# Performance work log

Hardware: AMD Instinct MI355X
Metric: run time of the kernel (lower is better)

## Reference

```python
import jax, jax.numpy as jnp
import numpy as np

N_NODES = 50000
N_EDGES = 1600000
F_IN = 256
OUT = 64
HEADS = 8


def setup_inputs() -> dict:
    key = jax.random.key(0)
    ks = jax.random.split(key, 6)
    x = jax.random.normal(ks[0], (N_NODES, F_IN), dtype=jnp.float32)
    edge_row = jax.random.randint(ks[1], (N_EDGES,), 0, N_NODES, dtype=jnp.int32)
    edge_col = jax.random.randint(ks[2], (N_EDGES,), 0, N_NODES, dtype=jnp.int32)
    Ws = jax.random.normal(ks[3], (HEADS, OUT, F_IN), dtype=jnp.float32) * (1.0 / np.sqrt(F_IN))
    Ws_bias = jnp.zeros((HEADS, OUT), dtype=jnp.float32)
    As = jax.random.normal(ks[4], (HEADS, 2 * OUT, 1), dtype=jnp.float32) * (1.0 / np.sqrt(OUT))
    As_bias = jnp.zeros((HEADS, 2), dtype=jnp.float32)
    return {"x": x, "edge_row": edge_row, "edge_col": edge_col,
            "Ws": Ws, "Ws_bias": Ws_bias, "As": As, "As_bias": As_bias}


def reference(x, edge_row, edge_col, Ws, Ws_bias, As, As_bias):
    # GAT forward, inference mode (training=False -> dropout rates 0).
    # Graph is a binary symmetric adjacency given as an edge list; the original's
    # sparse add of row_partial + transpose(col_partial) reduces to per-edge
    # score(i,j) = Al[i] + b0 + Ar[j] + b1 for every edge (i,j).
    # NOTE: the original computes leaky_relu(E) but then softmaxes E (lrelu is
    # discarded); we faithfully reproduce that: softmax over raw scores.
    H, O, F = Ws.shape
    N = x.shape[0]
    t = jnp.einsum('nf,hof->hno', x, Ws)                      # [H,N,O] transformed nodes
    Al = jnp.einsum('hno,ho->hn', t, As[:, :O, 0]) + As_bias[:, 0:1]  # [H,N]
    Ar = jnp.einsum('hno,ho->hn', t, As[:, O:, 0]) + As_bias[:, 1:2]  # [H,N]
    scores = Al[:, edge_row] + Ar[:, edge_col]                 # [H,E]
    seg_max = jax.vmap(lambda s: jax.ops.segment_max(s, edge_row, num_segments=N))(scores)
    seg_max = jnp.where(jnp.isfinite(seg_max), seg_max, jnp.float32(0.0))
    ex = jnp.exp(scores - seg_max[:, edge_row])                # [H,E]
    denom = jax.vmap(lambda e: jax.ops.segment_sum(e, edge_row, num_segments=N))(ex)
    alpha = ex / denom[:, edge_row]                            # row-wise sparse softmax
    # per-head aggregation (loop over small fixed head count bounds memory)
    h = jnp.stack([
        jax.ops.segment_sum(alpha[k][:, None] * t[k, edge_col, :], edge_row, num_segments=N)
        for k in range(H)
    ])                                                         # [H,N,O]
    h = h + Ws_bias[:, None, :]
    out = jnp.transpose(h, (1, 0, 2)).reshape(N, H * O)        # concat heads (reduction=False)
    return jax.nn.elu(out)
```

## Files before the change

### kernel.cpp

```cpp
#include <hip/hip_runtime.h>
#include <hip/hip_fp16.h>

#define HEADS 8
#define F_IN 256
#define OUT 64
#define NOUT 512
#define CAP 1024
#define CAPP (CAP + 16)

#define RPB 128
#define MAXB 512
#define CHA 8192

typedef __attribute__((ext_vector_type(8))) _Float16 f16x8;
typedef __attribute__((ext_vector_type(2))) _Float16 f16x2;
typedef __attribute__((ext_vector_type(4))) float f32x4;

__device__ __forceinline__ short f2h(float f) {
  _Float16 h = (_Float16)f;
  return *(short*)&h;
}
__device__ __forceinline__ f16x2 u2h2(unsigned u) {
  union { unsigned u; f16x2 h; } x; x.u = u; return x.h;
}
__device__ __forceinline__ float h2f(unsigned short b) {
  _Float16 h = *(_Float16*)&b; return (float)h;
}

__global__ __launch_bounds__(256) void conv_kernel(
    const float* __restrict__ src, short* __restrict__ dst, int n8)
{
  int i = blockIdx.x * 256 + threadIdx.x;
  if (i >= n8) return;
  const float4 a = *(const float4*)(src + (size_t)i * 8);
  const float4 b = *(const float4*)(src + (size_t)i * 8 + 4);
  short r[8] = { f2h(a.x), f2h(a.y), f2h(a.z), f2h(a.w),
                 f2h(b.x), f2h(b.y), f2h(b.z), f2h(b.w) };
  *(uint4*)(dst + (size_t)i * 8) = *(uint4*)r;
}

__global__ __launch_bounds__(256) void va_kernel(
    const short* __restrict__ W2, const float* __restrict__ As,
    unsigned short* __restrict__ va16)
{
  const int h = blockIdx.x, k = threadIdx.x;
  const unsigned short* W = (const unsigned short*)W2;
  float s = 0.f;
  #pragma unroll 8
  for (int o = 0; o < OUT; ++o)
    s += h2f(W[(size_t)(h * OUT + o) * F_IN + k]) * As[h * 2 * OUT + OUT + o];
  va16[h * F_IN + k] = (unsigned short)f2h(s);
}

__global__ __launch_bounds__(256) void argemv_kernel(
    const short* __restrict__ xh, const unsigned short* __restrict__ va16,
    const float* __restrict__ Asb, float* __restrict__ Wf, int N)
{
  __shared__ unsigned vas[8][132];
  for (int i = threadIdx.x; i < 1024; i += 256)
    vas[i >> 7][i & 127] = ((const unsigned*)va16)[i];
  __syncthreads();
  const int t = blockIdx.x * 256 + threadIdx.x;
  const int n = t >> 3, h = t & 7;
  if (n >= N) return;
  const unsigned short* xr = (const unsigned short*)xh + (size_t)n * F_IN;
  float acc = 0.f;
  #pragma unroll
  for (int kk = 0; kk < F_IN; kk += 8) {
    const uint4 xv = *(const uint4*)(xr + kk);
    const int p2 = kk >> 1;
    acc = __builtin_amdgcn_fdot2(u2h2(xv.x), u2h2(vas[h][p2]),     acc, false);
    acc = __builtin_amdgcn_fdot2(u2h2(xv.y), u2h2(vas[h][p2 + 1]), acc, false);
    acc = __builtin_amdgcn_fdot2(u2h2(xv.z), u2h2(vas[h][p2 + 2]), acc, false);
    acc = __builtin_amdgcn_fdot2(u2h2(xv.w), u2h2(vas[h][p2 + 3]), acc, false);
  }
  Wf[t] = __expf(acc + Asb[h * 2 + 1]);
}

__global__ __launch_bounds__(256) void gemm_mfma(
    const short* __restrict__ xh, const short* __restrict__ W2,
    const float* __restrict__ Wf, short* __restrict__ u, int N)
{
  __shared__ __align__(16) short as[128][72];
  __shared__ __align__(16) short bs[64][72];
  const int ytiles = (N + 127) / 128;
  const int YB = (ytiles + 7) / 8;
  const int bid = blockIdx.x;
  const int xcd = bid & 7;
  const int j   = bid >> 3;
  const int h   = j & 7;
  const int yt  = xcd * YB + (j >> 3);
  if (yt >= ytiles) return;
  const int n0 = yt * 128;
  const int NP1 = N + 1;
  const int tid = threadIdx.x;
  const int lane = tid & 63, wave = tid >> 6;
  const int lcol = lane & 15, quad = lane >> 4;
  const int m0 = wave * 32;
  const short* Wh = W2 + h * OUT * F_IN;

  f32x4 acc[2][4] = {};

  for (int k0 = 0; k0 < F_IN; k0 += 64) {
    __syncthreads();
    #pragma unroll
    for (int p = 0; p < 4; ++p) {
      int id = tid + 256 * p;
      int r = id >> 3, s = id & 7;
      int n = n0 + r;
      uint4 v = make_uint4(0, 0, 0, 0);
      if (n < N) v = *(const uint4*)(xh + (size_t)n * F_IN + k0 + s * 8);
      *(uint4*)&as[r][s * 8] = v;
    }
    #pragma unroll
    for (int p = 0; p < 2; ++p) {
      int id = tid + 256 * p;
      int r = id >> 3, s = id & 7;
      uint4 v = *(const uint4*)(Wh + r * F_IN + k0 + s * 8);
      *(uint4*)&bs[r][s * 8] = v;
    }
    __syncthreads();
    #pragma unroll
    for (int ks = 0; ks < 2; ++ks) {
      f16x8 af[2], bf[4];
      #pragma unroll
      for (int i = 0; i < 2; ++i)
        af[i] = *(const f16x8*)&as[m0 + i * 16 + lcol][ks * 32 + quad * 8];
      #pragma unroll
      for (int jj = 0; jj < 4; ++jj)
        bf[jj] = *(const f16x8*)&bs[jj * 16 + lcol][ks * 32 + quad * 8];
      #pragma unroll
      for (int i = 0; i < 2; ++i)
        #pragma unroll
        for (int jj = 0; jj < 4; ++jj)
          acc[i][jj] = __builtin_amdgcn_mfma_f32_16x16x32_f16(
              af[i], bf[jj], acc[i][jj], 0, 0, 0);
    }
  }

  #pragma unroll
  for (int i = 0; i < 2; ++i) {
    #pragma unroll
    for (int reg = 0; reg < 4; ++reg) {
      int n = n0 + m0 + i * 16 + quad * 4 + reg;
      if (n < N) {
        const float w = Wf[(size_t)n * 8 + h];
        #pragma unroll
        for (int jj = 0; jj < 4; ++jj) {
          const int hp = h * 2 + (jj >> 1);
          u[((size_t)hp * NP1 + n) * 32 + (jj & 1) * 16 + lcol] =
              f2h(acc[i][jj][reg] * w);
        }
      }
    }
  }
}

__global__ __launch_bounds__(64) void zdum_kernel(short* __restrict__ u, int N)
{
  const int t = threadIdx.x;
  const int hp = t >> 2, q = t & 3;
  *(uint4*)(u + ((size_t)hp * (N + 1) + N) * 32 + q * 8) = make_uint4(0, 0, 0, 0);
}

__global__ __launch_bounds__(256) void bcount_kernel(
    const int* __restrict__ row, int* __restrict__ bcnt, int E)
{
  __shared__ int h[MAXB];
  for (int i = threadIdx.x; i < MAXB; i += 256) h[i] = 0;
  __syncthreads();
  for (int e = blockIdx.x * 256 + threadIdx.x; e < E; e += gridDim.x * 256)
    atomicAdd(&h[row[e] >> 7], 1);
  __syncthreads();
  for (int i = threadIdx.x; i < MAXB; i += 256) {
    int v = h[i];
    if (v) atomicAdd(&bcnt[i], v);
  }
}

__global__ __launch_bounds__(MAXB) void bscan_kernel(
    const int* __restrict__ bcnt, int* __restrict__ bofs,
    int* __restrict__ gcur, int* __restrict__ rowptr_last, int E, int NB)
{
  __shared__ int sd[MAXB];
  const int t = threadIdx.x;
  int v = (t < NB) ? bcnt[t] : 0;
  sd[t] = v;
  __syncthreads();
  for (int off = 1; off < MAXB; off <<= 1) {
    int u = (t >= off) ? sd[t - off] : 0;
    __syncthreads();
    sd[t] += u;
    __syncthreads();
  }
  int excl = sd[t] - v;
  if (t < NB) { bofs[t] = excl; gcur[t] = excl; }
  if (t == NB - 1) bofs[NB] = excl + v;
  if (t == 0) rowptr_last[0] = E;
}

__global__ __launch_bounds__(256) void bscatter_kernel(
    const int* __restrict__ row, const int* __restrict__ col,
    int* __restrict__ gcur, unsigned* __restrict__ packed, int E)
{
  __shared__ int h[MAXB];
  __shared__ int base[MAXB];
  const int lo = blockIdx.x * CHA;
  const int hi = min(lo + CHA, E);
  for (int i = threadIdx.x; i < MAXB; i += 256) h[i] = 0;
  __syncthreads();
  for (int e = lo + threadIdx.x; e < hi; e += 256)
    atomicAdd(&h[row[e] >> 7], 1);
  __syncthreads();
  for (int i = threadIdx.x; i < MAXB; i += 256) {
    int v = h[i];
    base[i] = v ? atomicAdd(&gcur[i], v) : 0;
    h[i] = 0;
  }
  __syncthreads();
  for (int e = lo + threadIdx.x; e < hi; e += 256) {
    int r = row[e];
    int b = r >> 7;
    int p = base[b] + atomicAdd(&h[b], 1);
    packed[p] = ((unsigned)(r & (RPB - 1)) << 16) | (unsigned)col[e];
  }
}

__global__ __launch_bounds__(256) void bsort_kernel(
    const unsigned* __restrict__ packed, const int* __restrict__ bofs,
    int* __restrict__ row_ptr, int* __restrict__ col_sorted, int N)
{
  __shared__ int h[RPB];
  __shared__ int sd[RPB];
  __shared__ int cur[RPB];
  const int b = blockIdx.x;
  const int lo = bofs[b], hi = bofs[b + 1];
  const int t = threadIdx.x;
  if (t < RPB) h[t] = 0;
  __syncthreads();
  for (int i = lo + t; i < hi; i += 256)
    atomicAdd(&h[packed[i] >> 16], 1);
  __syncthreads();
  if (t < RPB) sd[t] = h[t];
  __syncthreads();
  for (int off = 1; off < RPB; off <<= 1) {
    int u = (t >= off && t < RPB) ? sd[t - off] : 0;
    __syncthreads();
    if (t < RPB) sd[t] += u;
    __syncthreads();
  }
  if (t < RPB) {
    int excl = sd[t] - h[t];
    cur[t] = lo + excl;
    int r = b * RPB + t;
    if (r < N) row_ptr[r] = lo + excl;
  }
  __syncthreads();
  for (int i = lo + t; i < hi; i += 256) {
    unsigned u = packed[i];
    int p = atomicAdd(&cur[u >> 16], 1);
    col_sorted[p] = (int)(u & 0xffffu);
  }
}

__global__ __launch_bounds__(256) void sw_kernel(
    const int* __restrict__ row_ptr, const int* __restrict__ col_sorted,
    const float* __restrict__ Wf, float* __restrict__ swb, int N)
{
  const int lane = threadIdx.x & 63;
  const int wave = threadIdx.x >> 6;
  const int row = blockIdx.x * 4 + wave;
  if (row >= N) return;
  const int start = row_ptr[row], end = row_ptr[row + 1];
  float a[8];
  #pragma unroll
  for (int i = 0; i < 8; ++i) a[i] = 0.f;
  for (int e = start + lane; e < end; e += 64) {
    int c = col_sorted[e];
    const float4 v0 = *(const float4*)(Wf + (size_t)c * 8);
    const float4 v1 = *(const float4*)(Wf + (size_t)c * 8 + 4);
    a[0] += v0.x; a[1] += v0.y; a[2] += v0.z; a[3] += v0.w;
    a[4] += v1.x; a[5] += v1.y; a[6] += v1.z; a[7] += v1.w;
  }
  #pragma unroll
  for (int off = 1; off <= 32; off <<= 1) {
    #pragma unroll
    for (int i = 0; i < 8; ++i) a[i] += __shfl_xor(a[i], off);
  }
  if (lane == 0) {
    float* sp = swb + (size_t)row * 8;
    *(float4*)sp       = make_float4(a[0], a[1], a[2], a[3]);
    *((float4*)sp + 1) = make_float4(a[4], a[5], a[6], a[7]);
  }
}

__global__ __launch_bounds__(256) void agg_kernel(
    const int* __restrict__ row_ptr, const int* __restrict__ col_sorted,
    const unsigned short* __restrict__ u, const float* __restrict__ swb,
    const float* __restrict__ Wb, float* __restrict__ out, int N, int p)
{
  __shared__ int ec[4][CAPP];
  const int lane = threadIdx.x & 63;
  const int wave = threadIdx.x >> 6;
  const int head = blockIdx.x & 7;
  const int g = lane >> 2, sub = lane & 3;
  const int rbase = ((blockIdx.x >> 3) * 4 + wave) * 16;
  const int row = rbase + g;
  const bool valid = row < N;
  const int NP1 = N + 1;

  const int wstart = row_ptr[min(rbase, N)];
  const int wend   = row_ptr[min(rbase + 16, N)];
  const int wlen = wend - wstart;
  const int nst = min(wlen, CAP);
  int* lds = ec[wave];
  for (int i = lane; i < nst; i += 64)
    lds[i] = __builtin_nontemporal_load(col_sorted + wstart + i);
  __syncthreads();

  const int sg = valid ? row_ptr[row]     : 0;
  const int eg = valid ? row_ptr[row + 1] : 0;
  const int deg = eg - sg;
  const unsigned short* ub =
      u + ((size_t)(head * 2 + p) * NP1) * 32 + (sub << 3);

  float acc[8];
  #pragma unroll
  for (int i = 0; i < 8; ++i) acc[i] = 0.f;
  const f16x2 ones = {(_Float16)1.0f, (_Float16)1.0f};

  if (wlen <= CAP) {
    const int lsg = valid ? sg - wstart : 0;
    const int nstg = (deg + 3) >> 2;
    const int nstg2 = max(2, (nstg + 1) & ~1);

    auto loadQ = [&](int s, int* c) {
      const int b = lsg + 4 * s;
      #pragma unroll
      for (int k = 0; k < 4; ++k) {
        int v = lds[b + k];
        c[k] = (4 * s + k < deg) ? v : N;
      }
    };
    auto issueQ = [&](const int* c, uint4* v) {
      #pragma unroll
      for (int k = 0; k < 4; ++k)
        v[k] = *(const uint4*)(ub + (size_t)c[k] * 32);
    };
    auto consumeQ = [&](const uint4* v) {
      #pragma unroll
      for (int pp = 0; pp < 2; ++pp) {
        unsigned a1[4] = { v[2*pp].x, v[2*pp].y, v[2*pp].z, v[2*pp].w };
        unsigned a2[4] = { v[2*pp+1].x, v[2*pp+1].y, v[2*pp+1].z, v[2*pp+1].w };
        #pragma unroll
        for (int q = 0; q < 4; ++q) {
          unsigned plo = __builtin_amdgcn_perm(a2[q], a1[q], 0x05040100u);
          unsigned phi = __builtin_amdgcn_perm(a2[q], a1[q], 0x07060302u);
          acc[2 * q]     = __builtin_amdgcn_fdot2(u2h2(plo), ones, acc[2 * q],     false);
          acc[2 * q + 1] = __builtin_amdgcn_fdot2(u2h2(phi), ones, acc[2 * q + 1], false);
        }
      }
    };

    int cA[4], cB[4];
    uint4 vA[4], vB[4];
    loadQ(0, cA); issueQ(cA, vA);
    loadQ(1, cB); issueQ(cB, vB);
    int s = 0;
    for (; s + 2 < nstg2; s += 2) {
      consumeQ(vA);
      loadQ(s + 2, cA); issueQ(cA, vA);
      consumeQ(vB);
      loadQ(s + 3, cB); issueQ(cB, vB);
    }
    consumeQ(vA);
    consumeQ(vB);
  } else {
    const int np = (deg + 1) >> 1;
    for (int j = 0; j < np; ++j) {
      const int e1 = sg + 2 * j, e2 = e1 + 1;
      const int c1 = (e1 < eg) ? __builtin_nontemporal_load(col_sorted + e1) : N;
      const int c2 = (e2 < eg) ? __builtin_nontemporal_load(col_sorted + e2) : N;
      const uint4 v1 = *(const uint4*)(ub + (size_t)c1 * 32);
      const uint4 v2 = *(const uint4*)(ub + (size_t)c2 * 32);
      unsigned a1[4] = { v1.x, v1.y, v1.z, v1.w };
      unsigned a2[4] = { v2.x, v2.y, v2.z, v2.w };
      #pragma unroll
      for (int q = 0; q < 4; ++q) {
        unsigned plo = __builtin_amdgcn_perm(a2[q], a1[q], 0x05040100u);
        unsigned phi = __builtin_amdgcn_perm(a2[q], a1[q], 0x07060302u);
        acc[2 * q]     = __builtin_amdgcn_fdot2(u2h2(plo), ones, acc[2 * q],     false);
        acc[2 * q + 1] = __builtin_amdgcn_fdot2(u2h2(phi), ones, acc[2 * q + 1], false);
      }
    }
  }

  if (valid) {
    const float sw = swb[(size_t)row * 8 + head];
    const float inv = (sw > 0.f) ? 1.f / sw : 0.f;
    const int bidx = head * OUT + p * 32 + (sub << 3);
    const float4 b0 = *(const float4*)(Wb + bidx);
    const float4 b1 = *(const float4*)(Wb + bidx + 4);
    const float bb[8] = { b0.x, b0.y, b0.z, b0.w, b1.x, b1.y, b1.z, b1.w };
    float r[8];
    #pragma unroll
    for (int i = 0; i < 8; ++i) {
      float y = acc[i] * inv + bb[i];
      r[i] = (y > 0.f) ? y : (__expf(y) - 1.f);
    }
    f32x4* op = (f32x4*)(out + (size_t)row * NOUT + bidx);
    f32x4 o0 = { r[0], r[1], r[2], r[3] };
    f32x4 o1 = { r[4], r[5], r[6], r[7] };
    __builtin_nontemporal_store(o0, op);
    __builtin_nontemporal_store(o1, op + 1);
  }
}

extern "C" void kernel_launch(void* const* d_in, const int* in_sizes, int n_in,
                              void* d_out, int out_size, void* d_ws, size_t ws_size,
                              hipStream_t stream)
{
  const float* x    = (const float*)d_in[0];
  const int*   erow = (const int*)d_in[1];
  const int*   ecol = (const int*)d_in[2];
  const float* Ws   = (const float*)d_in[3];
  const float* Wb   = (const float*)d_in[4];
  const float* As   = (const float*)d_in[5];
  const float* Asb  = (const float*)d_in[6];
  float* out = (float*)d_out;
  const int N = in_sizes[0] / F_IN;
  const int E = in_sizes[1];

  char* p = (char*)d_ws;
  short* u       = (short*)p; p += (size_t)16 * (N + 1) * 32 * sizeof(short);
  short* xh      = (short*)p; p += (size_t)N * F_IN * sizeof(short);
  short* W2      = (short*)p; p += (size_t)NOUT * F_IN * sizeof(short);
  unsigned short* va16 = (unsigned short*)p; p += (size_t)HEADS * F_IN * sizeof(short);
  float* Wf      = (float*)p; p += (size_t)N * HEADS * sizeof(float);
  float* swb     = (float*)p; p += (size_t)N * HEADS * sizeof(float);
  int* row_ptr   = (int*)p;   p += (size_t)(N + 1) * sizeof(int);
  int* bcnt      = (int*)p;   p += MAXB * sizeof(int);
  int* bofs      = (int*)p;   p += (MAXB + 1) * sizeof(int);
  int* gcur      = (int*)p;   p += MAXB * sizeof(int);
  int* col_sorted= (int*)p;   p += (size_t)E * sizeof(int);
  unsigned* packed = (unsigned*)u;

  const int NB = (N + RPB - 1) / RPB;

  (void)hipMemsetAsync(bcnt, 0, MAXB * sizeof(int), stream);

  bcount_kernel<<<dim3(512), dim3(256), 0, stream>>>(erow, bcnt, E);
  bscan_kernel<<<dim3(1), dim3(MAXB), 0, stream>>>(
      bcnt, bofs, gcur, row_ptr + N, E, NB);
  bscatter_kernel<<<dim3((E + CHA - 1) / CHA), dim3(256), 0, stream>>>(
      erow, ecol, gcur, packed, E);
  bsort_kernel<<<dim3(NB), dim3(256), 0, stream>>>(
      packed, bofs, row_ptr, col_sorted, N);
  zdum_kernel<<<dim3(1), dim3(64), 0, stream>>>(u, N);

  conv_kernel<<<dim3((N * F_IN / 8 + 255) / 256), dim3(256), 0, stream>>>(
      x, xh, N * F_IN / 8);
  conv_kernel<<<dim3((NOUT * F_IN / 8 + 255) / 256), dim3(256), 0, stream>>>(
      Ws, W2, NOUT * F_IN / 8);

  va_kernel<<<dim3(HEADS), dim3(F_IN), 0, stream>>>(W2, As, va16);
  argemv_kernel<<<dim3((N * HEADS + 255) / 256), dim3(256), 0, stream>>>(
      xh, va16, Asb, Wf, N);

  const int ytiles = (N + 127) / 128;
  const int YB = (ytiles + 7) / 8;
  gemm_mfma<<<dim3(8 * 8 * YB), dim3(256), 0, stream>>>(xh, W2, Wf, u, N);

  sw_kernel<<<dim3((N + 3) / 4), dim3(256), 0, stream>>>(
      row_ptr, col_sorted, Wf, swb, N);

  const int nblk = 8 * ((N + 63) / 64);
  agg_kernel<<<dim3(nblk), dim3(256), 0, stream>>>(
      row_ptr, col_sorted, (const unsigned short*)u, swb, Wb, out, N, 0);
  agg_kernel<<<dim3(nblk), dim3(256), 0, stream>>>(
      row_ptr, col_sorted, (const unsigned short*)u, swb, Wb, out, N, 1);
}
```

Before: 522.4 us.

## Fuse right-attention score computation into GEMM epilogue and shrink aggregation prefetch

```diff
diff --git a/kernel.cpp b/kernel.cpp
--- a/kernel.cpp
+++ b/kernel.cpp
@@ -39,47 +39,10 @@
   *(uint4*)(dst + (size_t)i * 8) = *(uint4*)r;
 }
 
-__global__ __launch_bounds__(256) void va_kernel(
-    const short* __restrict__ W2, const float* __restrict__ As,
-    unsigned short* __restrict__ va16)
-{
-  const int h = blockIdx.x, k = threadIdx.x;
-  const unsigned short* W = (const unsigned short*)W2;
-  float s = 0.f;
-  #pragma unroll 8
-  for (int o = 0; o < OUT; ++o)
-    s += h2f(W[(size_t)(h * OUT + o) * F_IN + k]) * As[h * 2 * OUT + OUT + o];
-  va16[h * F_IN + k] = (unsigned short)f2h(s);
-}
-
-__global__ __launch_bounds__(256) void argemv_kernel(
-    const short* __restrict__ xh, const unsigned short* __restrict__ va16,
-    const float* __restrict__ Asb, float* __restrict__ Wf, int N)
-{
-  __shared__ unsigned vas[8][132];
-  for (int i = threadIdx.x; i < 1024; i += 256)
-    vas[i >> 7][i & 127] = ((const unsigned*)va16)[i];
-  __syncthreads();
-  const int t = blockIdx.x * 256 + threadIdx.x;
-  const int n = t >> 3, h = t & 7;
-  if (n >= N) return;
-  const unsigned short* xr = (const unsigned short*)xh + (size_t)n * F_IN;
-  float acc = 0.f;
-  #pragma unroll
-  for (int kk = 0; kk < F_IN; kk += 8) {
-    const uint4 xv = *(const uint4*)(xr + kk);
-    const int p2 = kk >> 1;
-    acc = __builtin_amdgcn_fdot2(u2h2(xv.x), u2h2(vas[h][p2]),     acc, false);
-    acc = __builtin_amdgcn_fdot2(u2h2(xv.y), u2h2(vas[h][p2 + 1]), acc, false);
-    acc = __builtin_amdgcn_fdot2(u2h2(xv.z), u2h2(vas[h][p2 + 2]), acc, false);
-    acc = __builtin_amdgcn_fdot2(u2h2(xv.w), u2h2(vas[h][p2 + 3]), acc, false);
-  }
-  Wf[t] = __expf(acc + Asb[h * 2 + 1]);
-}
-
 __global__ __launch_bounds__(256) void gemm_mfma(
     const short* __restrict__ xh, const short* __restrict__ W2,
-    const float* __restrict__ Wf, short* __restrict__ u, int N)
+    const float* __restrict__ As, const float* __restrict__ Asb,
+    float* __restrict__ Wf, short* __restrict__ u, int N)
 {
   __shared__ __align__(16) short as[128][72];
   __shared__ __align__(16) short bs[64][72];
@@ -138,13 +101,23 @@
     }
   }
 
+  float arw_l[4];
+  #pragma unroll
+  for (int jj = 0; jj < 4; ++jj) arw_l[jj] = As[h * 2 * OUT + OUT + jj * 16 + lcol];
+  const float arb = Asb[h * 2 + 1];
   #pragma unroll
   for (int i = 0; i < 2; ++i) {
     #pragma unroll
     for (int reg = 0; reg < 4; ++reg) {
       int n = n0 + m0 + i * 16 + quad * 4 + reg;
+      float pr = 0.f;
+      #pragma unroll
+      for (int jj = 0; jj < 4; ++jj) pr = fmaf(acc[i][jj][reg], arw_l[jj], pr);
+      #pragma unroll
+      for (int off = 1; off < 16; off <<= 1) pr += __shfl_xor(pr, off);
+      const float w = __expf(pr + arb);
       if (n < N) {
-        const float w = Wf[(size_t)n * 8 + h];
+        if (lcol == 0) Wf[(size_t)n * 8 + h] = w;
         #pragma unroll
         for (int jj = 0; jj < 4; ++jj) {
           const int hp = h * 2 + (jj >> 1);
@@ -331,50 +304,44 @@
 
   if (wlen <= CAP) {
     const int lsg = valid ? sg - wstart : 0;
-    const int nstg = (deg + 3) >> 2;
-    const int nstg2 = max(2, (nstg + 1) & ~1);
-
-    auto loadQ = [&](int s, int* c) {
-      const int b = lsg + 4 * s;
-      #pragma unroll
-      for (int k = 0; k < 4; ++k) {
-        int v = lds[b + k];
-        c[k] = (4 * s + k < deg) ? v : N;
+    const int np = (deg + 1) >> 1;
+    const int nit2 = max(2, (np + 1) & ~1);
+
+    auto loadP = [&](int jj, int& c1, int& c2) {
+      const int b = lsg + 2 * jj;
+      const int v1 = lds[b], v2 = lds[b + 1];
+      c1 = (2 * jj     < deg) ? v1 : N;
+      c2 = (2 * jj + 1 < deg) ? v2 : N;
+    };
+    auto issueP = [&](int c1, int c2, uint4& v1, uint4& v2) {
+      v1 = *(const uint4*)(ub + (size_t)c1 * 32);
+      v2 = *(const uint4*)(ub + (size_t)c2 * 32);
+    };
+    auto consume = [&](const uint4& v1, const uint4& v2) {
+      unsigned a1[4] = { v1.x, v1.y, v1.z, v1.w };
+      unsigned a2[4] = { v2.x, v2.y, v2.z, v2.w };
+      #pragma unroll
+      for (int q = 0; q < 4; ++q) {
+        unsigned plo = __builtin_amdgcn_perm(a2[q], a1[q], 0x05040100u);
+        unsigned phi = __builtin_amdgcn_perm(a2[q], a1[q], 0x07060302u);
+        acc[2 * q]     = __builtin_amdgcn_fdot2(u2h2(plo), ones, acc[2 * q],     false);
+        acc[2 * q + 1] = __builtin_amdgcn_fdot2(u2h2(phi), ones, acc[2 * q + 1], false);
       }
     };
-    auto issueQ = [&](const int* c, uint4* v) {
-      #pragma unroll
-      for (int k = 0; k < 4; ++k)
-        v[k] = *(const uint4*)(ub + (size_t)c[k] * 32);
-    };
-    auto consumeQ = [&](const uint4* v) {
-      #pragma unroll
-      for (int pp = 0; pp < 2; ++pp) {
-        unsigned a1[4] = { v[2*pp].x, v[2*pp].y, v[2*pp].z, v[2*pp].w };
-        unsigned a2[4] = { v[2*pp+1].x, v[2*pp+1].y, v[2*pp+1].z, v[2*pp+1].w };
-        #pragma unroll
-        for (int q = 0; q < 4; ++q) {
-          unsigned plo = __builtin_amdgcn_perm(a2[q], a1[q], 0x05040100u);
-          unsigned phi = __builtin_amdgcn_perm(a2[q], a1[q], 0x07060302u);
-          acc[2 * q]     = __builtin_amdgcn_fdot2(u2h2(plo), ones, acc[2 * q],     false);
-          acc[2 * q + 1] = __builtin_amdgcn_fdot2(u2h2(phi), ones, acc[2 * q + 1], false);
-        }
-      }
-    };
-
-    int cA[4], cB[4];
-    uint4 vA[4], vB[4];
-    loadQ(0, cA); issueQ(cA, vA);
-    loadQ(1, cB); issueQ(cB, vB);
-    int s = 0;
-    for (; s + 2 < nstg2; s += 2) {
-      consumeQ(vA);
-      loadQ(s + 2, cA); issueQ(cA, vA);
-      consumeQ(vB);
-      loadQ(s + 3, cB); issueQ(cB, vB);
-    }
-    consumeQ(vA);
-    consumeQ(vB);
+
+    int cA1, cA2, cB1, cB2;
+    uint4 vA1, vA2, vB1, vB2;
+    loadP(0, cA1, cA2); issueP(cA1, cA2, vA1, vA2);
+    loadP(1, cB1, cB2); issueP(cB1, cB2, vB1, vB2);
+    int j = 0;
+    for (; j + 2 < nit2; j += 2) {
+      consume(vA1, vA2);
+      loadP(j + 2, cA1, cA2); issueP(cA1, cA2, vA1, vA2);
+      consume(vB1, vB2);
+      loadP(j + 3, cB1, cB2); issueP(cB1, cB2, vB1, vB2);
+    }
+    consume(vA1, vA2);
+    consume(vB1, vB2);
   } else {
     const int np = (deg + 1) >> 1;
     for (int j = 0; j < np; ++j) {
@@ -435,7 +402,6 @@
   short* u       = (short*)p; p += (size_t)16 * (N + 1) * 32 * sizeof(short);
   short* xh      = (short*)p; p += (size_t)N * F_IN * sizeof(short);
   short* W2      = (short*)p; p += (size_t)NOUT * F_IN * sizeof(short);
-  unsigned short* va16 = (unsigned short*)p; p += (size_t)HEADS * F_IN * sizeof(short);
   float* Wf      = (float*)p; p += (size_t)N * HEADS * sizeof(float);
   float* swb     = (float*)p; p += (size_t)N * HEADS * sizeof(float);
   int* row_ptr   = (int*)p;   p += (size_t)(N + 1) * sizeof(int);
@@ -463,13 +429,10 @@
   conv_kernel<<<dim3((NOUT * F_IN / 8 + 255) / 256), dim3(256), 0, stream>>>(
       Ws, W2, NOUT * F_IN / 8);
 
-  va_kernel<<<dim3(HEADS), dim3(F_IN), 0, stream>>>(W2, As, va16);
-  argemv_kernel<<<dim3((N * HEADS + 255) / 256), dim3(256), 0, stream>>>(
-      xh, va16, Asb, Wf, N);
-
   const int ytiles = (N + 127) / 128;
   const int YB = (ytiles + 7) / 8;
-  gemm_mfma<<<dim3(8 * 8 * YB), dim3(256), 0, stream>>>(xh, W2, Wf, u, N);
+  gemm_mfma<<<dim3(8 * 8 * YB), dim3(256), 0, stream>>>(
+      xh, W2, As, Asb, Wf, u, N);
 
   sw_kernel<<<dim3((N + 3) / 4), dim3(256), 0, stream>>>(
       row_ptr, col_sorted, Wf, swb, N);
```

New measurement: 486.9 us. -6.8%, faster.
